# Optimization experiments

Hardware: AMD Instinct MI355X
Metric: run time of the kernel (lower is better)

## Reference

```python
import jax, jax.numpy as jnp
import numpy as np

N_NODES = 50000
N_EDGES = 800000
D_IN = 128
D_OUT = 128
BN_EPS = 1e-5


def setup_inputs() -> dict:
    key = jax.random.key(0)
    ks = jax.random.split(key, 8)
    node_feats = jax.random.normal(ks[0], (N_NODES, D_IN), dtype=jnp.float32)
    src = jax.random.randint(ks[1], (N_EDGES,), 0, N_NODES, dtype=jnp.int32)
    dst = jax.random.randint(ks[2], (N_EDGES,), 0, N_NODES, dtype=jnp.int32)
    # Glorot-ish init for weights
    scale = 1.0 / np.sqrt(D_IN)
    W = jax.random.normal(ks[3], (D_IN, D_OUT), dtype=jnp.float32) * scale
    b = jnp.zeros((D_OUT,), dtype=jnp.float32)
    Wr = jax.random.normal(ks[4], (D_IN, D_OUT), dtype=jnp.float32) * scale
    br = jnp.zeros((D_OUT,), dtype=jnp.float32)
    gamma = jnp.ones((D_OUT,), dtype=jnp.float32)
    beta = jnp.zeros((D_OUT,), dtype=jnp.float32)
    return {"node_feats": node_feats, "src": src, "dst": dst, "W": W, "b": b,
            "Wr": Wr, "br": br, "gamma": gamma, "beta": beta}


def reference(node_feats, src, dst, W, b, Wr, br, gamma, beta):
    N = node_feats.shape[0]
    ones_e = jnp.ones(src.shape[0], dtype=node_feats.dtype)
    # DGL GraphConv norm='both': D_out^{-1/2} on source side, D_in^{-1/2} on dest side
    deg_out = jnp.clip(jax.ops.segment_sum(ones_e, src, num_segments=N), 1.0)
    deg_in = jnp.clip(jax.ops.segment_sum(ones_e, dst, num_segments=N), 1.0)
    h = node_feats * jax.lax.rsqrt(deg_out)[:, None]        # [N, D_in]
    agg = jax.ops.segment_sum(h[src], dst, num_segments=N)  # gather + scatter-add, [N, D_in]
    agg = agg * jax.lax.rsqrt(deg_in)[:, None]
    gcn = jax.nn.relu(agg @ W + b)                           # GraphConv activation=relu
    res = jax.nn.relu(node_feats @ Wr + br)                  # residual branch
    y = gcn + res
    # BatchNorm1d (training mode: biased batch stats)
    mean = jnp.mean(y, axis=0)
    var = jnp.mean(jnp.square(y - mean), axis=0)
    out = (y - mean) * jax.lax.rsqrt(var + BN_EPS) * gamma + beta
    return out
```

## Files before the change

kernel.cpp:

```cpp
#include <hip/hip_runtime.h>

#define N_NODES 50000
#define N_EDGES 800000
#define D 128
#define BN_EPS 1e-5f
#define AGG_BLOCKS 2048
#define SCAN_BLOCKS 196
#define CHUNKS 64
#define EPC (N_EDGES / CHUNKS)
#define HALF_BINS 25600
#define HALF_U32 12800

typedef short bf16x8 __attribute__((ext_vector_type(8)));
typedef float f32x4  __attribute__((ext_vector_type(4)));
typedef unsigned int u32x4 __attribute__((ext_vector_type(4)));


__global__ __launch_bounds__(256) void hist_kernel(
        const int* __restrict__ dst, const int* __restrict__ src,
        unsigned int* __restrict__ histD, unsigned int* __restrict__ histS) {
    __shared__ unsigned int h[HALF_U32];
    int tid = threadIdx.x;
    int c = blockIdx.x, r = blockIdx.y;
    const int* keys = blockIdx.z ? src : dst;
    unsigned int* hist = blockIdx.z ? histS : histD;
    for (int j = tid; j < HALF_U32; j += 256) h[j] = 0u;
    __syncthreads();
    int base = c * EPC;
    int lo = r * HALF_BINS;
    for (int i = tid; i < EPC; i += 256) {
        int b = keys[base + i] - lo;
        if ((unsigned)b < (unsigned)HALF_BINS)
            atomicAdd(&h[b >> 1], 1u << ((b & 1) * 16));
    }
    __syncthreads();
    unsigned int* out = hist + ((size_t)(r * CHUNKS + c)) * HALF_U32;
    for (int j = tid; j < HALF_U32; j += 256) out[j] = h[j];
}

__global__ __launch_bounds__(256) void merge_kernel(
        unsigned int* __restrict__ histD, unsigned int* __restrict__ histS,
        int* __restrict__ cnt_in, int* __restrict__ cnt_out) {
    int q = blockIdx.x * 256 + threadIdx.x;
    int r = blockIdx.y;
    unsigned int* hist = blockIdx.z ? histS : histD;
    int* cnt = blockIdx.z ? cnt_out : cnt_in;
    unsigned int lo = 0, hi = 0;
    for (int c = 0; c < CHUNKS; c++) {
        size_t idx = ((size_t)(r * CHUNKS + c)) * HALF_U32 + q;
        unsigned int v = hist[idx];
        hist[idx] = lo | (hi << 16);
        lo += v & 0xffffu; hi += v >> 16;
    }
    int n0 = r * HALF_BINS + q * 2;
    cnt[n0]     = (int)lo;
    cnt[n0 + 1] = (int)hi;
}

__global__ __launch_bounds__(256) void scan1_kernel(
        const int* __restrict__ cnt_in, int* __restrict__ row_ptr, int* __restrict__ blk_sum) {
    __shared__ int sh[256];
    int t = threadIdx.x;
    int i = blockIdx.x * 256 + t;
    int v = cnt_in[i];
    sh[t] = v;
    __syncthreads();
    int inc = v;
    #pragma unroll
    for (int off = 1; off < 256; off <<= 1) {
        int u = (t >= off) ? sh[t - off] : 0;
        __syncthreads();
        inc += u; sh[t] = inc;
        __syncthreads();
    }
    row_ptr[i] = inc - v;
    if (t == 255) blk_sum[blockIdx.x] = inc;
}

__global__ __launch_bounds__(256) void scan2_kernel(int* __restrict__ blk_sum, int* __restrict__ row_ptr) {
    __shared__ int sh[256];
    int t = threadIdx.x;
    int v = (t < SCAN_BLOCKS) ? blk_sum[t] : 0;
    sh[t] = v;
    __syncthreads();
    int inc = v;
    #pragma unroll
    for (int off = 1; off < 256; off <<= 1) {
        int u = (t >= off) ? sh[t - off] : 0;
        __syncthreads();
        inc += u; sh[t] = inc;
        __syncthreads();
    }
    if (t < SCAN_BLOCKS) blk_sum[t] = inc - v;
    if (t == 0) row_ptr[N_NODES] = N_EDGES;
}

__global__ __launch_bounds__(256) void scan3_kernel(
        const int* __restrict__ cnt_in, const int* __restrict__ cnt_out,
        const int* __restrict__ blk_sum, int* __restrict__ row_ptr,
        float* __restrict__ rin, float* __restrict__ rout) {
    int i = blockIdx.x * 256 + threadIdx.x;
    if (i < N_NODES) {
        row_ptr[i] = row_ptr[i] + blk_sum[blockIdx.x];
        int ci = cnt_in[i], co = cnt_out[i];
        rin[i]  = rsqrtf((float)(ci > 1 ? ci : 1));
        rout[i] = rsqrtf((float)(co > 1 ? co : 1));
    }
}

__global__ __launch_bounds__(512) void fill2_kernel(
        const int* __restrict__ src, const int* __restrict__ dst,
        const int* __restrict__ row_ptr, const unsigned int* __restrict__ histP,
        int* __restrict__ csr_src) {
    __shared__ unsigned int h[HALF_U32];
    int tid = threadIdx.x;
    int c = blockIdx.x;
    int base = c * EPC;
    for (int r = 0; r < 2; r++) {
        for (int j = tid; j < HALF_U32; j += 512) h[j] = 0u;
        __syncthreads();
        int lo = r * HALF_BINS;
        const unsigned int* pre_c = histP + ((size_t)(r * CHUNKS + c)) * HALF_U32;
        for (int i = tid; i < EPC; i += 512) {
            int d = dst[base + i];
            int b = d - lo;
            if ((unsigned)b < (unsigned)HALF_BINS) {
                int sh = (b & 1) * 16;
                unsigned int old = atomicAdd(&h[b >> 1], 1u << sh);
                unsigned int rank = (old >> sh) & 0xffffu;
                unsigned int pre = (pre_c[b >> 1] >> sh) & 0xffffu;
                int p = row_ptr[d] + (int)(pre + rank);
                csr_src[p] = src[base + i];
            }
        }
        __syncthreads();
    }
}

__device__ __forceinline__ unsigned int pack_rne(float a, float b) {
    unsigned int ua = __float_as_uint(a); ua += 0x7fffu + ((ua >> 16) & 1u);
    unsigned int ub = __float_as_uint(b); ub += 0x7fffu + ((ub >> 16) & 1u);
    return (ua >> 16) | (ub & 0xffff0000u);
}
__device__ __forceinline__ unsigned short pack1_rne(float a) {
    unsigned int ua = __float_as_uint(a); ua += 0x7fffu + ((ua >> 16) & 1u);
    return (unsigned short)(ua >> 16);
}

__global__ __launch_bounds__(256) void pack_w(
        const float* __restrict__ W, const float* __restrict__ Wr,
        uint4* __restrict__ pW, uint4* __restrict__ pWr) {
    int t = blockIdx.x * 256 + threadIdx.x;
    const float* S = (t & 2048) ? Wr : W;
    uint4* Dst     = (t & 2048) ? pWr : pW;
    int e = t & 2047;
    int lane = e & 63, ks = (e >> 6) & 3, ct = e >> 8;
    int n  = ct * 16 + (lane & 15);
    int k0 = ks * 32 + (lane >> 4) * 8;
    float v[8];
    #pragma unroll
    for (int j = 0; j < 8; j++) v[j] = S[(k0 + j) * D + n];
    uint4 r;
    r.x = pack_rne(v[0], v[1]); r.y = pack_rne(v[2], v[3]);
    r.z = pack_rne(v[4], v[5]); r.w = pack_rne(v[6], v[7]);
    Dst[e] = r;
}

__global__ __launch_bounds__(256) void gemm_mfma(
        const float* __restrict__ x, const uint4* __restrict__ pW,
        const uint4* __restrict__ pWr, const float* __restrict__ br,
        const float* __restrict__ rout, unsigned short* __restrict__ hwb,
        unsigned short* __restrict__ resb) {
    __shared__ unsigned short xs[64][136];
    int tid = threadIdx.x, wid = tid >> 6, lane = tid & 63;
    int quad = lane >> 4, l15 = lane & 15;
    int r0b = blockIdx.x * 64;
    const float4* xg = (const float4*)(x + (size_t)r0b * D);
    int maxidx = (N_NODES - r0b) * (D / 4);
    #pragma unroll
    for (int i = 0; i < 8; i++) {
        int idx = tid + 256 * i;
        float4 v = (idx < maxidx) ? xg[idx] : make_float4(0.f, 0.f, 0.f, 0.f);
        int row = idx >> 5, c0 = (idx & 31) * 4;
        *(unsigned int*)&xs[row][c0]     = pack_rne(v.x, v.y);
        *(unsigned int*)&xs[row][c0 + 2] = pack_rne(v.z, v.w);
    }
    __syncthreads();
    int wrow0 = wid * 16;
    bf16x8 A[4];
    #pragma unroll
    for (int ks = 0; ks < 4; ks++)
        A[ks] = *(const bf16x8*)&xs[wrow0 + l15][ks * 32 + quad * 8];
    f32x4 accW[8], accR[8];
    #pragma unroll
    for (int ct = 0; ct < 8; ct++) { accW[ct] = (f32x4)0.f; accR[ct] = (f32x4)0.f; }
    #pragma unroll
    for (int ct = 0; ct < 8; ct++) {
        #pragma unroll
        for (int ks = 0; ks < 4; ks++) {
            union { bf16x8 v; uint4 u; } Bw, Br2;
            Bw.u  = pW [(ct * 4 + ks) * 64 + lane];
            Br2.u = pWr[(ct * 4 + ks) * 64 + lane];
            accW[ct] = __builtin_amdgcn_mfma_f32_16x16x32_bf16(A[ks], Bw.v,  accW[ct], 0, 0, 0);
            accR[ct] = __builtin_amdgcn_mfma_f32_16x16x32_bf16(A[ks], Br2.v, accR[ct], 0, 0, 0);
        }
    }
    int r0 = r0b + wrow0;
    float ro[4]; int rowok[4];
    #pragma unroll
    for (int reg = 0; reg < 4; reg++) {
        int row = r0 + quad * 4 + reg;
        rowok[reg] = row < N_NODES;
        ro[reg] = rout[rowok[reg] ? row : N_NODES - 1];
    }
    #pragma unroll
    for (int ct = 0; ct < 8; ct++) {
        int c = ct * 16 + l15;
        float brv = br[c];
        #pragma unroll
        for (int reg = 0; reg < 4; reg++) {
            int row = r0 + quad * 4 + reg;
            if (rowok[reg]) {
                hwb [(size_t)row * D + c] = pack1_rne(accW[ct][reg] * ro[reg]);
                resb[(size_t)row * D + c] = pack1_rne(fmaxf(accR[ct][reg] + brv, 0.f));
            }
        }
    }
}

__device__ __forceinline__ float bf_lo(unsigned int v) { return __uint_as_float(v << 16); }
__device__ __forceinline__ float bf_hi(unsigned int v) { return __uint_as_float(v & 0xffff0000u); }

__device__ __forceinline__ void acc8(float* a, const uint4 v) {
    a[0] += bf_lo(v.x); a[1] += bf_hi(v.x);
    a[2] += bf_lo(v.y); a[3] += bf_hi(v.y);
    a[4] += bf_lo(v.z); a[5] += bf_hi(v.z);
    a[6] += bf_lo(v.w); a[7] += bf_hi(v.w);
}
__device__ __forceinline__ void acc8m(float* a, const uint4 v, float m) {
    a[0] = fmaf(m, bf_lo(v.x), a[0]); a[1] = fmaf(m, bf_hi(v.x), a[1]);
    a[2] = fmaf(m, bf_lo(v.y), a[2]); a[3] = fmaf(m, bf_hi(v.y), a[3]);
    a[4] = fmaf(m, bf_lo(v.z), a[4]); a[5] = fmaf(m, bf_hi(v.z), a[5]);
    a[6] = fmaf(m, bf_lo(v.w), a[6]); a[7] = fmaf(m, bf_hi(v.w), a[7]);
}

__device__ __forceinline__ int sel4(int qg, int i0, int i1, int i2, int i3) {
    int a = (qg & 1) ? i1 : i0;
    int b = (qg & 1) ? i3 : i2;
    return (qg & 2) ? b : a;
}

__global__ __launch_bounds__(256) void agg_kernel(
        const unsigned int* __restrict__ hwb, const int* __restrict__ row_ptr,
        const int* __restrict__ csr_src, const float* __restrict__ rin,
        const float* __restrict__ bias, const unsigned short* __restrict__ resb,
        float* __restrict__ y, float* __restrict__ parts) {
    __shared__ float red[4 * 256];
    int tid = threadIdx.x;
    int lane = tid & 63, wid = tid >> 6;
    int wave = blockIdx.x * 4 + wid;
    int nw = AGG_BLOCKS * 4;
    int qg = lane >> 4;
    int ql = lane & 15;
    float s1[8] = {0,0,0,0,0,0,0,0}, s2[8] = {0,0,0,0,0,0,0,0};
    float4 bv0, bv1;
    if (lane < 16) {
        bv0 = ((const float4*)bias)[2 * lane];
        bv1 = ((const float4*)bias)[2 * lane + 1];
    }
    for (int n = wave; n < N_NODES; n += nw) {
        int e0 = row_ptr[n], e1 = row_ptr[n + 1];
        u32x4 rv4 = (u32x4)0u;
        if (lane < 16)
            rv4 = __builtin_nontemporal_load((const u32x4*)(resb + (size_t)n * D) + lane);
        float a[8] = {0,0,0,0,0,0,0,0};
        for (int j0 = e0; j0 < e1; j0 += 64) {
            int cnt = e1 - j0; if (cnt > 64) cnt = 64;
            int myidx = (lane < cnt) ? __builtin_nontemporal_load(csr_src + j0 + lane) : 0;
            int i = 0;
            for (; i + 16 <= cnt; i += 16) {
                int p0 = sel4(qg, __builtin_amdgcn_readlane(myidx, i + 0),
                                  __builtin_amdgcn_readlane(myidx, i + 1),
                                  __builtin_amdgcn_readlane(myidx, i + 2),
                                  __builtin_amdgcn_readlane(myidx, i + 3));
                int p1 = sel4(qg, __builtin_amdgcn_readlane(myidx, i + 4),
                                  __builtin_amdgcn_readlane(myidx, i + 5),
                                  __builtin_amdgcn_readlane(myidx, i + 6),
                                  __builtin_amdgcn_readlane(myidx, i + 7));
                int p2 = sel4(qg, __builtin_amdgcn_readlane(myidx, i + 8),
                                  __builtin_amdgcn_readlane(myidx, i + 9),
                                  __builtin_amdgcn_readlane(myidx, i + 10),
                                  __builtin_amdgcn_readlane(myidx, i + 11));
                int p3 = sel4(qg, __builtin_amdgcn_readlane(myidx, i + 12),
                                  __builtin_amdgcn_readlane(myidx, i + 13),
                                  __builtin_amdgcn_readlane(myidx, i + 14),
                                  __builtin_amdgcn_readlane(myidx, i + 15));
                uint4 v0 = *((const uint4*)(hwb + (size_t)p0 * 64) + ql);
                uint4 v1 = *((const uint4*)(hwb + (size_t)p1 * 64) + ql);
                uint4 v2 = *((const uint4*)(hwb + (size_t)p2 * 64) + ql);
                uint4 v3 = *((const uint4*)(hwb + (size_t)p3 * 64) + ql);
                acc8(a, v0); acc8(a, v1); acc8(a, v2); acc8(a, v3);
            }
            for (; i + 4 <= cnt; i += 4) {
                int p0 = sel4(qg, __builtin_amdgcn_readlane(myidx, i + 0),
                                  __builtin_amdgcn_readlane(myidx, i + 1),
                                  __builtin_amdgcn_readlane(myidx, i + 2),
                                  __builtin_amdgcn_readlane(myidx, i + 3));
                uint4 v0 = *((const uint4*)(hwb + (size_t)p0 * 64) + ql);
                acc8(a, v0);
            }
            int t = cnt - i;
            if (t > 0) {
                int lim = cnt - 1;
                int j1 = i + 1 <= lim ? i + 1 : lim;
                int j2 = i + 2 <= lim ? i + 2 : lim;
                int p0 = sel4(qg, __builtin_amdgcn_readlane(myidx, i),
                                  __builtin_amdgcn_readlane(myidx, j1),
                                  __builtin_amdgcn_readlane(myidx, j2),
                                  __builtin_amdgcn_readlane(myidx, lim));
                uint4 v0 = *((const uint4*)(hwb + (size_t)p0 * 64) + ql);
                float m = (qg < t) ? 1.f : 0.f;
                acc8m(a, v0, m);
            }
        }
        #pragma unroll
        for (int k = 0; k < 8; k++) {
            a[k] += __shfl_xor(a[k], 16);
            a[k] += __shfl_xor(a[k], 32);
        }
        if (lane < 16) {
            float ri = rin[n];
            float o[8];
            o[0] = fmaxf(a[0] * ri + bv0.x, 0.f) + bf_lo(rv4.x);
            o[1] = fmaxf(a[1] * ri + bv0.y, 0.f) + bf_hi(rv4.x);
            o[2] = fmaxf(a[2] * ri + bv0.z, 0.f) + bf_lo(rv4.y);
            o[3] = fmaxf(a[3] * ri + bv0.w, 0.f) + bf_hi(rv4.y);
            o[4] = fmaxf(a[4] * ri + bv1.x, 0.f) + bf_lo(rv4.z);
            o[5] = fmaxf(a[5] * ri + bv1.y, 0.f) + bf_hi(rv4.z);
            o[6] = fmaxf(a[6] * ri + bv1.z, 0.f) + bf_lo(rv4.w);
            o[7] = fmaxf(a[7] * ri + bv1.w, 0.f) + bf_hi(rv4.w);
            float4* yv = (float4*)(y + (size_t)n * D);
            yv[2 * lane]     = make_float4(o[0], o[1], o[2], o[3]);
            yv[2 * lane + 1] = make_float4(o[4], o[5], o[6], o[7]);
            #pragma unroll
            for (int k = 0; k < 8; k++) { s1[k] += o[k]; s2[k] += o[k] * o[k]; }
        }
    }
    if (lane < 16) {
        int c0 = lane * 8;
        #pragma unroll
        for (int k = 0; k < 8; k++) {
            red[wid * 256 + c0 + k]       = s1[k];
            red[wid * 256 + 128 + c0 + k] = s2[k];
        }
    }
    __syncthreads();
    if (tid < 256) {
        float v = red[tid] + red[256 + tid] + red[512 + tid] + red[768 + tid];
        parts[(size_t)blockIdx.x * 256 + tid] = v;
    }
}

__global__ __launch_bounds__(256) void bn_fin2(
        const float* __restrict__ parts, const float* __restrict__ gamma,
        const float* __restrict__ beta, float* __restrict__ scsh) {
    __shared__ float rs1[256], rs2[256];
    int c = blockIdx.x, t = threadIdx.x;
    float s1 = 0.f, s2 = 0.f;
    for (int b = t; b < AGG_BLOCKS; b += 256) {
        s1 += parts[(size_t)b * 256 + c];
        s2 += parts[(size_t)b * 256 + 128 + c];
    }
    rs1[t] = s1; rs2[t] = s2;
    __syncthreads();
    for (int off = 128; off > 0; off >>= 1) {
        if (t < off) { rs1[t] += rs1[t + off]; rs2[t] += rs2[t + off]; }
        __syncthreads();
    }
    if (t == 0) {
        const float invN = 1.0f / (float)N_NODES;
        float mean = rs1[0] * invN;
        float var  = rs2[0] * invN - mean * mean;
        float sc = gamma[c] * rsqrtf(var + BN_EPS);
        scsh[c] = sc;
        scsh[128 + c] = beta[c] - mean * sc;
    }
}

__global__ void norm_kernel(float* __restrict__ y, const float* __restrict__ scsh) {
    int i = blockIdx.x * blockDim.x + threadIdx.x;
    if (i < N_NODES * 32) {
        float4 v = ((float4*)y)[i];
        int c = (i & 31) * 4;
        v.x = v.x * scsh[c]     + scsh[128 + c];
        v.y = v.y * scsh[c + 1] + scsh[128 + c + 1];
        v.z = v.z * scsh[c + 2] + scsh[128 + c + 2];
        v.w = v.w * scsh[c + 3] + scsh[128 + c + 3];
        ((float4*)y)[i] = v;
    }
}

extern "C" void kernel_launch(void* const* d_in, const int* in_sizes, int n_in,
                              void* d_out, int out_size, void* d_ws, size_t ws_size,
                              hipStream_t stream) {
    const float* x     = (const float*)d_in[0];
    const int*   src   = (const int*)d_in[1];
    const int*   dst   = (const int*)d_in[2];
    const float* W     = (const float*)d_in[3];
    const float* b     = (const float*)d_in[4];
    const float* Wr    = (const float*)d_in[5];
    const float* br    = (const float*)d_in[6];
    const float* gamma = (const float*)d_in[7];
    const float* beta  = (const float*)d_in[8];
    float* out = (float*)d_out;

    char* ws = (char*)d_ws;
    int*   cnt_in  = (int*)(ws + 0);
    int*   cnt_out = (int*)(ws + 262144);
    int*   row_ptr = (int*)(ws + 524288);
    float* rin     = (float*)(ws + 1048576);
    float* rout    = (float*)(ws + 1310720);
    float* scsh    = (float*)(ws + 1576960);
    int*   blk_sum = (int*)(ws + 1579008);
    int*   csr_src = (int*)(ws + 1581056);
    unsigned short* hwb = (unsigned short*)(ws + 4800000);
    float* parts   = (float*)(ws + 17600000);
    uint4* pW      = (uint4*)(ws + 19697152);
    uint4* pWr     = (uint4*)(ws + 19729920);
    unsigned int* histD = (unsigned int*)(ws + 19762688);
    unsigned int* histS = (unsigned int*)(ws + 26316288);
    unsigned short* resb = (unsigned short*)(ws + 19762688);

    hist_kernel<<<dim3(CHUNKS, 2, 2), 256, 0, stream>>>(dst, src, histD, histS);
    merge_kernel<<<dim3(HALF_U32 / 256, 2, 2), 256, 0, stream>>>(histD, histS, cnt_in, cnt_out);
    scan1_kernel<<<SCAN_BLOCKS, 256, 0, stream>>>(cnt_in, row_ptr, blk_sum);
    scan2_kernel<<<1, 256, 0, stream>>>(blk_sum, row_ptr);
    scan3_kernel<<<SCAN_BLOCKS, 256, 0, stream>>>(cnt_in, cnt_out, blk_sum, row_ptr, rin, rout);
    fill2_kernel<<<CHUNKS, 512, 0, stream>>>(src, dst, row_ptr, histD, csr_src);
    pack_w<<<16, 256, 0, stream>>>(W, Wr, pW, pWr);
    gemm_mfma<<<(N_NODES + 63) / 64, 256, 0, stream>>>(x, pW, pWr, br, rout, hwb, resb);
    agg_kernel<<<AGG_BLOCKS, 256, 0, stream>>>((const unsigned int*)hwb, row_ptr, csr_src, rin, b, resb, out, parts);
    bn_fin2<<<128, 256, 0, stream>>>(parts, gamma, beta, scsh);
    norm_kernel<<<(N_NODES * 32 + 255) / 256, 256, 0, stream>>>(out, scsh);
}
```

Baseline: 246.4 us.

## Fold weight packing and block-scan into existing kernels, prefetch next node in aggregation

Result: faster. 239.0 us (-3.0%).

```diff
diff --git a/kernel.cpp b/kernel.cpp
--- a/kernel.cpp
+++ b/kernel.cpp
@@ -16,12 +16,42 @@
 typedef unsigned int u32x4 __attribute__((ext_vector_type(4)));
 
 
+__device__ __forceinline__ unsigned int pack_rne(float a, float b) {
+    unsigned int ua = __float_as_uint(a); ua += 0x7fffu + ((ua >> 16) & 1u);
+    unsigned int ub = __float_as_uint(b); ub += 0x7fffu + ((ub >> 16) & 1u);
+    return (ua >> 16) | (ub & 0xffff0000u);
+}
+__device__ __forceinline__ unsigned short pack1_rne(float a) {
+    unsigned int ua = __float_as_uint(a); ua += 0x7fffu + ((ua >> 16) & 1u);
+    return (unsigned short)(ua >> 16);
+}
+
 __global__ __launch_bounds__(256) void hist_kernel(
         const int* __restrict__ dst, const int* __restrict__ src,
-        unsigned int* __restrict__ histD, unsigned int* __restrict__ histS) {
+        unsigned int* __restrict__ histD, unsigned int* __restrict__ histS,
+        const float* __restrict__ W, const float* __restrict__ Wr,
+        uint4* __restrict__ pW, uint4* __restrict__ pWr) {
     __shared__ unsigned int h[HALF_U32];
     int tid = threadIdx.x;
     int c = blockIdx.x, r = blockIdx.y;
+    if (c >= CHUNKS) {
+        if (r != 0 || blockIdx.z != 0) return;
+        int t = (c - CHUNKS) * 256 + tid;
+        const float* S = (t & 2048) ? Wr : W;
+        uint4* Dst     = (t & 2048) ? pWr : pW;
+        int e = t & 2047;
+        int lane = e & 63, ks = (e >> 6) & 3, ct = e >> 8;
+        int n  = ct * 16 + (lane & 15);
+        int k0 = ks * 32 + (lane >> 4) * 8;
+        float v[8];
+        #pragma unroll
+        for (int j = 0; j < 8; j++) v[j] = S[(k0 + j) * D + n];
+        uint4 rr;
+        rr.x = pack_rne(v[0], v[1]); rr.y = pack_rne(v[2], v[3]);
+        rr.z = pack_rne(v[4], v[5]); rr.w = pack_rne(v[6], v[7]);
+        Dst[e] = rr;
+        return;
+    }
     const int* keys = blockIdx.z ? src : dst;
     unsigned int* hist = blockIdx.z ? histS : histD;
     for (int j = tid; j < HALF_U32; j += 256) h[j] = 0u;
@@ -77,7 +107,10 @@
     if (t == 255) blk_sum[blockIdx.x] = inc;
 }
 
-__global__ __launch_bounds__(256) void scan2_kernel(int* __restrict__ blk_sum, int* __restrict__ row_ptr) {
+__global__ __launch_bounds__(256) void scan3_kernel(
+        const int* __restrict__ cnt_in, const int* __restrict__ cnt_out,
+        const int* __restrict__ blk_sum, int* __restrict__ row_ptr,
+        float* __restrict__ rin, float* __restrict__ rout) {
     __shared__ int sh[256];
     int t = threadIdx.x;
     int v = (t < SCAN_BLOCKS) ? blk_sum[t] : 0;
@@ -91,21 +124,15 @@
         inc += u; sh[t] = inc;
         __syncthreads();
     }
-    if (t < SCAN_BLOCKS) blk_sum[t] = inc - v;
-    if (t == 0) row_ptr[N_NODES] = N_EDGES;
-}
-
-__global__ __launch_bounds__(256) void scan3_kernel(
-        const int* __restrict__ cnt_in, const int* __restrict__ cnt_out,
-        const int* __restrict__ blk_sum, int* __restrict__ row_ptr,
-        float* __restrict__ rin, float* __restrict__ rout) {
-    int i = blockIdx.x * 256 + threadIdx.x;
+    int boff = (blockIdx.x == 0) ? 0 : sh[blockIdx.x - 1];
+    int i = blockIdx.x * 256 + t;
     if (i < N_NODES) {
-        row_ptr[i] = row_ptr[i] + blk_sum[blockIdx.x];
+        row_ptr[i] = row_ptr[i] + boff;
         int ci = cnt_in[i], co = cnt_out[i];
         rin[i]  = rsqrtf((float)(ci > 1 ? ci : 1));
         rout[i] = rsqrtf((float)(co > 1 ? co : 1));
     }
+    if (blockIdx.x == SCAN_BLOCKS - 1 && t == 0) row_ptr[N_NODES] = N_EDGES;
 }
 
 __global__ __launch_bounds__(512) void fill2_kernel(
@@ -137,35 +164,6 @@
     }
 }
 
-__device__ __forceinline__ unsigned int pack_rne(float a, float b) {
-    unsigned int ua = __float_as_uint(a); ua += 0x7fffu + ((ua >> 16) & 1u);
-    unsigned int ub = __float_as_uint(b); ub += 0x7fffu + ((ub >> 16) & 1u);
-    return (ua >> 16) | (ub & 0xffff0000u);
-}
-__device__ __forceinline__ unsigned short pack1_rne(float a) {
-    unsigned int ua = __float_as_uint(a); ua += 0x7fffu + ((ua >> 16) & 1u);
-    return (unsigned short)(ua >> 16);
-}
-
-__global__ __launch_bounds__(256) void pack_w(
-        const float* __restrict__ W, const float* __restrict__ Wr,
-        uint4* __restrict__ pW, uint4* __restrict__ pWr) {
-    int t = blockIdx.x * 256 + threadIdx.x;
-    const float* S = (t & 2048) ? Wr : W;
-    uint4* Dst     = (t & 2048) ? pWr : pW;
-    int e = t & 2047;
-    int lane = e & 63, ks = (e >> 6) & 3, ct = e >> 8;
-    int n  = ct * 16 + (lane & 15);
-    int k0 = ks * 32 + (lane >> 4) * 8;
-    float v[8];
-    #pragma unroll
-    for (int j = 0; j < 8; j++) v[j] = S[(k0 + j) * D + n];
-    uint4 r;
-    r.x = pack_rne(v[0], v[1]); r.y = pack_rne(v[2], v[3]);
-    r.z = pack_rne(v[4], v[5]); r.w = pack_rne(v[6], v[7]);
-    Dst[e] = r;
-}
-
 __global__ __launch_bounds__(256) void gemm_mfma(
         const float* __restrict__ x, const uint4* __restrict__ pW,
         const uint4* __restrict__ pWr, const float* __restrict__ br,
@@ -248,6 +246,56 @@
     int a = (qg & 1) ? i1 : i0;
     int b = (qg & 1) ? i3 : i2;
     return (qg & 2) ? b : a;
+}
+
+__device__ __forceinline__ void gather_accum(
+        const unsigned int* __restrict__ hwb, int myidx, int cnt,
+        int qg, int ql, float* a) {
+    int i = 0;
+    for (; i + 16 <= cnt; i += 16) {
+        int p0 = sel4(qg, __builtin_amdgcn_readlane(myidx, i + 0),
+                          __builtin_amdgcn_readlane(myidx, i + 1),
+                          __builtin_amdgcn_readlane(myidx, i + 2),
+                          __builtin_amdgcn_readlane(myidx, i + 3));
+        int p1 = sel4(qg, __builtin_amdgcn_readlane(myidx, i + 4),
+                          __builtin_amdgcn_readlane(myidx, i + 5),
+                          __builtin_amdgcn_readlane(myidx, i + 6),
+                          __builtin_amdgcn_readlane(myidx, i + 7));
+        int p2 = sel4(qg, __builtin_amdgcn_readlane(myidx, i + 8),
+                          __builtin_amdgcn_readlane(myidx, i + 9),
+                          __builtin_amdgcn_readlane(myidx, i + 10),
+                          __builtin_amdgcn_readlane(myidx, i + 11));
+        int p3 = sel4(qg, __builtin_amdgcn_readlane(myidx, i + 12),
+                          __builtin_amdgcn_readlane(myidx, i + 13),
+                          __builtin_amdgcn_readlane(myidx, i + 14),
+                          __builtin_amdgcn_readlane(myidx, i + 15));
+        uint4 v0 = *((const uint4*)(hwb + (size_t)p0 * 64) + ql);
+        uint4 v1 = *((const uint4*)(hwb + (size_t)p1 * 64) + ql);
+        uint4 v2 = *((const uint4*)(hwb + (size_t)p2 * 64) + ql);
+        uint4 v3 = *((const uint4*)(hwb + (size_t)p3 * 64) + ql);
+        acc8(a, v0); acc8(a, v1); acc8(a, v2); acc8(a, v3);
+    }
+    for (; i + 4 <= cnt; i += 4) {
+        int p0 = sel4(qg, __builtin_amdgcn_readlane(myidx, i + 0),
+                          __builtin_amdgcn_readlane(myidx, i + 1),
+                          __builtin_amdgcn_readlane(myidx, i + 2),
+                          __builtin_amdgcn_readlane(myidx, i + 3));
+        uint4 v0 = *((const uint4*)(hwb + (size_t)p0 * 64) + ql);
+        acc8(a, v0);
+    }
+    int t = cnt - i;
+    if (t > 0) {
+        int lim = cnt - 1;
+        int j1 = i + 1 <= lim ? i + 1 : lim;
+        int j2 = i + 2 <= lim ? i + 2 : lim;
+        int p0 = sel4(qg, __builtin_amdgcn_readlane(myidx, i),
+                          __builtin_amdgcn_readlane(myidx, j1),
+                          __builtin_amdgcn_readlane(myidx, j2),
+                          __builtin_amdgcn_readlane(myidx, lim));
+        uint4 v0 = *((const uint4*)(hwb + (size_t)p0 * 64) + ql);
+        float m = (qg < t) ? 1.f : 0.f;
+        acc8m(a, v0, m);
+    }
 }
 
 __global__ __launch_bounds__(256) void agg_kernel(
@@ -268,60 +316,38 @@
         bv0 = ((const float4*)bias)[2 * lane];
         bv1 = ((const float4*)bias)[2 * lane + 1];
     }
-    for (int n = wave; n < N_NODES; n += nw) {
-        int e0 = row_ptr[n], e1 = row_ptr[n + 1];
-        u32x4 rv4 = (u32x4)0u;
-        if (lane < 16)
-            rv4 = __builtin_nontemporal_load((const u32x4*)(resb + (size_t)n * D) + lane);
+    int n = wave;
+    int e0 = 0, e1 = 0, mi = 0;
+    u32x4 rv4 = (u32x4)0u;
+    float ri = 0.f;
+    if (n < N_NODES) {
+        e0 = row_ptr[n]; e1 = row_ptr[n + 1];
+        ri = rin[n];
+        if (lane < 16) rv4 = __builtin_nontemporal_load((const u32x4*)(resb + (size_t)n * D) + lane);
+        int c0 = e1 - e0; if (c0 > 64) c0 = 64;
+        mi = (lane < c0) ? __builtin_nontemporal_load(csr_src + e0 + lane) : 0;
+    }
+    while (n < N_NODES) {
+        int nn = n + nw;
+        int ne0 = 0, ne1 = 0, nmi = 0;
+        u32x4 nrv = (u32x4)0u;
+        float nri = 0.f;
+        if (nn < N_NODES) {
+            ne0 = row_ptr[nn]; ne1 = row_ptr[nn + 1];
+            nri = rin[nn];
+            if (lane < 16) nrv = __builtin_nontemporal_load((const u32x4*)(resb + (size_t)nn * D) + lane);
+            int nc = ne1 - ne0; if (nc > 64) nc = 64;
+            nmi = (lane < nc) ? __builtin_nontemporal_load(csr_src + ne0 + lane) : 0;
+        }
         float a[8] = {0,0,0,0,0,0,0,0};
-        for (int j0 = e0; j0 < e1; j0 += 64) {
+        {
+            int cnt = e1 - e0; if (cnt > 64) cnt = 64;
+            gather_accum(hwb, mi, cnt, qg, ql, a);
+        }
+        for (int j0 = e0 + 64; j0 < e1; j0 += 64) {
             int cnt = e1 - j0; if (cnt > 64) cnt = 64;
-            int myidx = (lane < cnt) ? __builtin_nontemporal_load(csr_src + j0 + lane) : 0;
-            int i = 0;
-            for (; i + 16 <= cnt; i += 16) {
-                int p0 = sel4(qg, __builtin_amdgcn_readlane(myidx, i + 0),
-                                  __builtin_amdgcn_readlane(myidx, i + 1),
-                                  __builtin_amdgcn_readlane(myidx, i + 2),
-                                  __builtin_amdgcn_readlane(myidx, i + 3));
-                int p1 = sel4(qg, __builtin_amdgcn_readlane(myidx, i + 4),
-                                  __builtin_amdgcn_readlane(myidx, i + 5),
-                                  __builtin_amdgcn_readlane(myidx, i + 6),
-                                  __builtin_amdgcn_readlane(myidx, i + 7));
-                int p2 = sel4(qg, __builtin_amdgcn_readlane(myidx, i + 8),
-                                  __builtin_amdgcn_readlane(myidx, i + 9),
-                                  __builtin_amdgcn_readlane(myidx, i + 10),
-                                  __builtin_amdgcn_readlane(myidx, i + 11));
-                int p3 = sel4(qg, __builtin_amdgcn_readlane(myidx, i + 12),
-                                  __builtin_amdgcn_readlane(myidx, i + 13),
-                                  __builtin_amdgcn_readlane(myidx, i + 14),
-                                  __builtin_amdgcn_readlane(myidx, i + 15));
-                uint4 v0 = *((const uint4*)(hwb + (size_t)p0 * 64) + ql);
-                uint4 v1 = *((const uint4*)(hwb + (size_t)p1 * 64) + ql);
-                uint4 v2 = *((const uint4*)(hwb + (size_t)p2 * 64) + ql);
-                uint4 v3 = *((const uint4*)(hwb + (size_t)p3 * 64) + ql);
-                acc8(a, v0); acc8(a, v1); acc8(a, v2); acc8(a, v3);
-            }
-            for (; i + 4 <= cnt; i += 4) {
-                int p0 = sel4(qg, __builtin_amdgcn_readlane(myidx, i + 0),
-                                  __builtin_amdgcn_readlane(myidx, i + 1),
-                                  __builtin_amdgcn_readlane(myidx, i + 2),
-                                  __builtin_amdgcn_readlane(myidx, i + 3));
-                uint4 v0 = *((const uint4*)(hwb + (size_t)p0 * 64) + ql);
-                acc8(a, v0);
-            }
-            int t = cnt - i;
-            if (t > 0) {
-                int lim = cnt - 1;
-                int j1 = i + 1 <= lim ? i + 1 : lim;
-                int j2 = i + 2 <= lim ? i + 2 : lim;
-                int p0 = sel4(qg, __builtin_amdgcn_readlane(myidx, i),
-                                  __builtin_amdgcn_readlane(myidx, j1),
-                                  __builtin_amdgcn_readlane(myidx, j2),
-                                  __builtin_amdgcn_readlane(myidx, lim));
-                uint4 v0 = *((const uint4*)(hwb + (size_t)p0 * 64) + ql);
-                float m = (qg < t) ? 1.f : 0.f;
-                acc8m(a, v0, m);
-            }
+            int mw = (lane < cnt) ? __builtin_nontemporal_load(csr_src + j0 + lane) : 0;
+            gather_accum(hwb, mw, cnt, qg, ql, a);
         }
         #pragma unroll
         for (int k = 0; k < 8; k++) {
@@ -329,7 +355,6 @@
             a[k] += __shfl_xor(a[k], 32);
         }
         if (lane < 16) {
-            float ri = rin[n];
             float o[8];
             o[0] = fmaxf(a[0] * ri + bv0.x, 0.f) + bf_lo(rv4.x);
             o[1] = fmaxf(a[1] * ri + bv0.y, 0.f) + bf_hi(rv4.x);
@@ -345,6 +370,7 @@
             #pragma unroll
             for (int k = 0; k < 8; k++) { s1[k] += o[k]; s2[k] += o[k] * o[k]; }
         }
+        n = nn; e0 = ne0; e1 = ne1; mi = nmi; rv4 = nrv; ri = nri;
     }
     if (lane < 16) {
         int c0 = lane * 8;
@@ -431,13 +457,11 @@
     unsigned int* histS = (unsigned int*)(ws + 26316288);
     unsigned short* resb = (unsigned short*)(ws + 19762688);
 
-    hist_kernel<<<dim3(CHUNKS, 2, 2), 256, 0, stream>>>(dst, src, histD, histS);
+    hist_kernel<<<dim3(CHUNKS + 16, 2, 2), 256, 0, stream>>>(dst, src, histD, histS, W, Wr, pW, pWr);
     merge_kernel<<<dim3(HALF_U32 / 256, 2, 2), 256, 0, stream>>>(histD, histS, cnt_in, cnt_out);
     scan1_kernel<<<SCAN_BLOCKS, 256, 0, stream>>>(cnt_in, row_ptr, blk_sum);
-    scan2_kernel<<<1, 256, 0, stream>>>(blk_sum, row_ptr);
     scan3_kernel<<<SCAN_BLOCKS, 256, 0, stream>>>(cnt_in, cnt_out, blk_sum, row_ptr, rin, rout);
     fill2_kernel<<<CHUNKS, 512, 0, stream>>>(src, dst, row_ptr, histD, csr_src);
-    pack_w<<<16, 256, 0, stream>>>(W, Wr, pW, pWr);
     gemm_mfma<<<(N_NODES + 63) / 64, 256, 0, stream>>>(x, pW, pWr, br, rout, hwb, resb);
     agg_kernel<<<AGG_BLOCKS, 256, 0, stream>>>((const unsigned int*)hwb, row_ptr, csr_src, rin, b, resb, out, parts);
     bn_fin2<<<128, 256, 0, stream>>>(parts, gamma, beta, scsh);
```
